# Performance work log

Measured on AMD Instinct MI355X. Metric: run time of the kernel, lower is better.

## Reference

```python
import jax, jax.numpy as jnp
import numpy as np

N, IN_DIM, OUT_DIM, H = 4096, 128, 128, 4
HEAD_DIM = OUT_DIM // H
NEG_SLOPE = 0.2


def setup_inputs() -> dict:
    key = jax.random.key(0)
    k1, k2, k3, k4, k5 = jax.random.split(key, 5)
    x = jax.random.normal(k1, (N, IN_DIM), dtype=jnp.float32)
    adj = jax.random.randint(k2, (N, N), 0, 2, dtype=jnp.int32)
    # nn.Linear(in_dim, out_dim, bias=False): weight is [out_dim, in_dim]
    W = jax.random.normal(k3, (OUT_DIM, IN_DIM), dtype=jnp.float32) * (1.0 / np.sqrt(IN_DIM))
    attn_src = jax.random.normal(k4, (1, H, HEAD_DIM), dtype=jnp.float32) * 0.1
    attn_dst = jax.random.normal(k5, (1, H, HEAD_DIM), dtype=jnp.float32) * 0.1
    return {"x": x, "adj": adj, "W": W, "attn_src": attn_src, "attn_dst": attn_dst}


def reference(x, adj, W, attn_src, attn_dst):
    n = x.shape[0]
    h = (x @ W.T).reshape(n, H, HEAD_DIM)            # [N, H, D]
    e_src = jnp.sum(h * attn_src, axis=-1)           # [N, H]
    e_dst = jnp.sum(h * attn_dst, axis=-1)           # [N, H]
    e = e_src[:, None, :] + e_dst[None, :, :]        # [N, N, H]
    e = jax.nn.leaky_relu(e, negative_slope=NEG_SLOPE)
    e = jnp.where((adj == 0)[:, :, None], -jnp.inf, e)
    alpha = jax.nn.softmax(e, axis=1)                # softmax over neighbors j
    # dropout omitted (eval mode)
    out = jnp.einsum('ijh,jhd->ihd', alpha, h)       # [N, H, D]
    return out.reshape(n, -1)
```

## Files before the change

kernel.cpp:

```cpp
#include <hip/hip_runtime.h>
#include <hip/hip_bf16.h>

#define NN 4096
#define SJ 8
#define JCH (NN / SJ)
#define JSTEP 64
#define NSTEPS (JCH / JSTEP)
#define LOG2E 1.44269504f

typedef __attribute__((ext_vector_type(4))) float f32x4;
typedef __attribute__((ext_vector_type(4))) int i32x4;
typedef __attribute__((ext_vector_type(4))) unsigned int u32x4;
typedef __attribute__((ext_vector_type(8))) short short8;

__device__ __forceinline__ unsigned pk2(float a, float b) {
    float2 t; t.x = a; t.y = b;
    __hip_bfloat162 h = __float22bfloat162_rn(t);
    unsigned r;
    __builtin_memcpy(&r, &h, 4);
    return r;
}

__device__ __forceinline__ short8 load8_bf(const float* __restrict__ p) {
    f32x4 a = *(const f32x4*)p;
    f32x4 b = *(const f32x4*)(p + 4);
    u32x4 v = {pk2(a[0], a[1]), pk2(a[2], a[3]), pk2(b[0], b[1]), pk2(b[2], b[3])};
    return __builtin_bit_cast(short8, v);
}

__global__ __launch_bounds__(256) void k1_proj(
        const float* __restrict__ x, const float* __restrict__ W,
        const float* __restrict__ asrc, const float* __restrict__ adst,
        unsigned short* __restrict__ hT, float* __restrict__ esT,
        float* __restrict__ edT) {
    const int ibase = blockIdx.x * 16;
    const int w = threadIdx.x >> 6;
    const int lane = threadIdx.x & 63;
    const int grp = lane >> 4, li = lane & 15;

    const float* xrow = x + (ibase + li) * 128;
    const float* w0 = W + (w * 32 + li) * 128;
    const float* w1 = W + (w * 32 + 16 + li) * 128;

    f32x4 c0 = {0.f, 0.f, 0.f, 0.f}, c1 = {0.f, 0.f, 0.f, 0.f};
#pragma unroll
    for (int ko = 0; ko < 128; ko += 32) {
        const int kk = ko + grp * 8;
        short8 a = load8_bf(xrow + kk);
        short8 b0 = load8_bf(w0 + kk);
        short8 b1 = load8_bf(w1 + kk);
        c0 = __builtin_amdgcn_mfma_f32_16x16x32_bf16(a, b0, c0, 0, 0, 0);
        c1 = __builtin_amdgcn_mfma_f32_16x16x32_bf16(a, b1, c1, 0, 0, 0);
    }
    const float as0 = asrc[w * 32 + li], as1 = asrc[w * 32 + 16 + li];
    const float ad0 = adst[w * 32 + li], ad1 = adst[w * 32 + 16 + li];
    float pes[4], ped[4];
#pragma unroll
    for (int r = 0; r < 4; ++r) {
        pes[r] = c0[r] * as0 + c1[r] * as1;
        ped[r] = c0[r] * ad0 + c1[r] * ad1;
    }
#pragma unroll
    for (int m = 1; m < 16; m <<= 1) {
#pragma unroll
        for (int r = 0; r < 4; ++r) {
            pes[r] += __shfl_xor(pes[r], m);
            ped[r] += __shfl_xor(ped[r], m);
        }
    }
    if (li == 0) {
#pragma unroll
        for (int r = 0; r < 4; ++r) {
            const int row = ibase + grp * 4 + r;
            esT[w * NN + row] = pes[r] * LOG2E;
            edT[w * NN + row] = ped[r] * LOG2E;
        }
    }
#pragma unroll
    for (int r = 0; r < 4; ++r) {
        const int row = ibase + grp * 4 + r;
        hT[(w * 32 + li) * NN + row] = (unsigned short)__builtin_bit_cast(unsigned short, __float2bfloat16(c0[r]));
        hT[(w * 32 + 16 + li) * NN + row] = (unsigned short)__builtin_bit_cast(unsigned short, __float2bfloat16(c1[r]));
    }
}

__device__ __forceinline__ short8 buildA(float es, const f32x4 edlo, const f32x4 edhi,
                                         const i32x4 alo, const i32x4 ahi) {
    float p[8];
#pragma unroll
    for (int e = 0; e < 4; ++e) {
        float s = es + edlo[e];
        float v = __builtin_amdgcn_exp2f(fmaxf(s, 0.2f * s));
        p[e] = (alo[e] != 0) ? v : 0.0f;
    }
#pragma unroll
    for (int e = 0; e < 4; ++e) {
        float s = es + edhi[e];
        float v = __builtin_amdgcn_exp2f(fmaxf(s, 0.2f * s));
        p[4 + e] = (ahi[e] != 0) ? v : 0.0f;
    }
    u32x4 u = {pk2(p[0], p[1]), pk2(p[2], p[3]), pk2(p[4], p[5]), pk2(p[6], p[7])};
    return __builtin_bit_cast(short8, u);
}

__global__ __launch_bounds__(256) void k3_main(
        const int* __restrict__ adj, const unsigned short* __restrict__ hT,
        const float* __restrict__ esT, const float* __restrict__ edT,
        float* __restrict__ numer, float* __restrict__ denom) {
    __shared__ unsigned int adjbuf[2][32 * 64];

    const int ibase = blockIdx.x * 32;
    const int jstart = blockIdx.y * JCH;
    const int head = threadIdx.x >> 6;
    const int lane = threadIdx.x & 63;
    const int grp = lane >> 4, li = lane & 15;
    const int sub = lane >> 4, p = lane & 15;

    const float es0 = esT[head * NN + ibase + li];
    const float es1 = esT[head * NN + ibase + 16 + li];
    const float* edp = edT + head * NN;
    const unsigned short* h0 = hT + (head * 32 + li) * NN;
    const unsigned short* h1 = hT + (head * 32 + 16 + li) * NN;
    const unsigned int* adju = (const unsigned int*)adj;

    f32x4 c00 = {0.f,0.f,0.f,0.f}, c01 = {0.f,0.f,0.f,0.f};
    f32x4 c10 = {0.f,0.f,0.f,0.f}, c11 = {0.f,0.f,0.f,0.f};
    f32x4 dn0 = {0.f,0.f,0.f,0.f}, dn1 = {0.f,0.f,0.f,0.f};
    short8 bones;
#pragma unroll
    for (int e = 0; e < 8; ++e) bones[e] = (short)0x3F80;

    auto stage = [&](unsigned int* dst, int jb) {
#pragma unroll
        for (int k = 0; k < 2; ++k) {
            const int R = head * 8 + k * 4 + sub;
            const int c = p ^ (R & 15);
            const unsigned int* g = adju + (size_t)(ibase + R) * NN + jb + c * 4;
            __builtin_amdgcn_global_load_lds(g, dst + (head * 8 + k * 4) * 64, 16, 0, 0);
        }
    };

    unsigned int* cur = &adjbuf[0][0];
    unsigned int* nxt = &adjbuf[1][0];

    stage(cur, jstart);
    __syncthreads();

    for (int t = 0; t < NSTEPS; ++t) {
        const int jb = jstart + t * JSTEP;
        if (t + 1 < NSTEPS) stage(nxt, jb + JSTEP);

#pragma unroll
        for (int ks = 0; ks < 2; ++ks) {
            const int j0 = jb + ks * 32 + grp * 8;
            const f32x4 e0 = *(const f32x4*)(edp + j0);
            const f32x4 e1 = *(const f32x4*)(edp + j0 + 4);
            const short8 b0 = *(const short8*)(h0 + j0);
            const short8 b1 = *(const short8*)(h1 + j0);

            const int c0i = ks * 8 + grp * 2;
            const i32x4 q00 = *(const i32x4*)&cur[li * 64 + (c0i ^ li) * 4];
            const i32x4 q01 = *(const i32x4*)&cur[li * 64 + ((c0i + 1) ^ li) * 4];
            const i32x4 q10 = *(const i32x4*)&cur[(li + 16) * 64 + (c0i ^ li) * 4];
            const i32x4 q11 = *(const i32x4*)&cur[(li + 16) * 64 + ((c0i + 1) ^ li) * 4];

            const short8 A0 = buildA(es0, e0, e1, q00, q01);
            const short8 A1 = buildA(es1, e0, e1, q10, q11);

            c00 = __builtin_amdgcn_mfma_f32_16x16x32_bf16(A0, b0, c00, 0, 0, 0);
            c01 = __builtin_amdgcn_mfma_f32_16x16x32_bf16(A0, b1, c01, 0, 0, 0);
            c10 = __builtin_amdgcn_mfma_f32_16x16x32_bf16(A1, b0, c10, 0, 0, 0);
            c11 = __builtin_amdgcn_mfma_f32_16x16x32_bf16(A1, b1, c11, 0, 0, 0);
            dn0 = __builtin_amdgcn_mfma_f32_16x16x32_bf16(A0, bones, dn0, 0, 0, 0);
            dn1 = __builtin_amdgcn_mfma_f32_16x16x32_bf16(A1, bones, dn1, 0, 0, 0);
        }

        __syncthreads();
        unsigned int* tmp = cur; cur = nxt; nxt = tmp;
    }

    const int r0 = ibase + grp * 4;
    float* nb = numer + head * 32 + li;
#pragma unroll
    for (int r = 0; r < 4; ++r) {
        atomicAdd(nb + (size_t)(r0 + r) * 128, c00[r]);
        atomicAdd(nb + (size_t)(r0 + r) * 128 + 16, c01[r]);
        atomicAdd(nb + (size_t)(r0 + 16 + r) * 128, c10[r]);
        atomicAdd(nb + (size_t)(r0 + 16 + r) * 128 + 16, c11[r]);
    }
    if (li == 0) {
#pragma unroll
        for (int r = 0; r < 4; ++r) {
            atomicAdd(denom + (r0 + r) * 4 + head, dn0[r]);
            atomicAdd(denom + (r0 + 16 + r) * 4 + head, dn1[r]);
        }
    }
}

__global__ __launch_bounds__(256) void k4_fin(const float* __restrict__ numer,
                                              const float* __restrict__ denom,
                                              float* __restrict__ out) {
    const int idx = blockIdx.x * 256 + threadIdx.x;
    const int node = idx >> 7;
    const int headc = (idx & 127) >> 5;
    out[idx] = numer[idx] / denom[node * 4 + headc];
}

extern "C" void kernel_launch(void* const* d_in, const int* in_sizes, int n_in,
                              void* d_out, int out_size, void* d_ws, size_t ws_size,
                              hipStream_t stream) {
    const float* x = (const float*)d_in[0];
    const int* adj = (const int*)d_in[1];
    const float* W = (const float*)d_in[2];
    const float* asrc = (const float*)d_in[3];
    const float* adst = (const float*)d_in[4];
    float* out = (float*)d_out;

    char* ws = (char*)d_ws;
    float* numer = (float*)ws;
    float* denom = (float*)(ws + (size_t)2097152);
    float* esT = (float*)(ws + (size_t)2097152 + 65536);
    float* edT = (float*)(ws + (size_t)2097152 + 131072);
    unsigned short* hT = (unsigned short*)(ws + (size_t)2097152 + 196608);

    (void)hipMemsetAsync(numer, 0, 2097152 + 65536, stream);
    k1_proj<<<256, 256, 0, stream>>>(x, W, asrc, adst, hT, esT, edT);
    k3_main<<<dim3(128, SJ), 256, 0, stream>>>(adj, hT, esT, edT, numer, denom);
    k4_fin<<<2048, 256, 0, stream>>>(numer, denom, out);
}
```

Measured before the change: 59.36 us.

## Factor leaky-relu exponent into per-node exp terms, remove per-edge exp2

The per-edge exp2(leaky(es+ed)) becomes max(exp(ed), exp(-0.8 es) * exp(0.2 ed)) multiplied by a row scale. This relies on exp being monotone, and the softmax ratio cancels the constant factor exp(es). The exponentials are computed once per node in the projection kernel, so the inner loop does one multiply, one max and a bitmask select in place of an exp. The adjacency select becomes a bit-AND mask. The j-split also doubles to 16 and occupancy is hinted at 6 waves. In exchange there are extra loads of two per-node arrays, more atomics, and possible overflow or underflow, since exp values are not shifted by a running max.

```diff
diff --git a/kernel.cpp b/kernel.cpp
--- a/kernel.cpp
+++ b/kernel.cpp
@@ -2,7 +2,7 @@
 #include <hip/hip_bf16.h>
 
 #define NN 4096
-#define SJ 8
+#define SJ 16
 #define JCH (NN / SJ)
 #define JSTEP 64
 #define NSTEPS (JCH / JSTEP)
@@ -31,8 +31,8 @@
 __global__ __launch_bounds__(256) void k1_proj(
         const float* __restrict__ x, const float* __restrict__ W,
         const float* __restrict__ asrc, const float* __restrict__ adst,
-        unsigned short* __restrict__ hT, float* __restrict__ esT,
-        float* __restrict__ edT) {
+        unsigned short* __restrict__ hT, float* __restrict__ Rt,
+        float* __restrict__ Bt, float* __restrict__ Dt) {
     const int ibase = blockIdx.x * 16;
     const int w = threadIdx.x >> 6;
     const int lane = threadIdx.x & 63;
@@ -72,8 +72,9 @@
 #pragma unroll
         for (int r = 0; r < 4; ++r) {
             const int row = ibase + grp * 4 + r;
-            esT[w * NN + row] = pes[r] * LOG2E;
-            edT[w * NN + row] = ped[r] * LOG2E;
+            Rt[w * NN + row] = __builtin_amdgcn_exp2f(-0.8f * LOG2E * pes[r]);
+            Bt[w * NN + row] = __builtin_amdgcn_exp2f(LOG2E * ped[r]);
+            Dt[w * NN + row] = __builtin_amdgcn_exp2f(0.2f * LOG2E * ped[r]);
         }
     }
 #pragma unroll
@@ -84,28 +85,31 @@
     }
 }
 
-__device__ __forceinline__ short8 buildA(float es, const f32x4 edlo, const f32x4 edhi,
+__device__ __forceinline__ short8 buildQ(float R,
+                                         const f32x4 B0, const f32x4 B1,
+                                         const f32x4 D0, const f32x4 D1,
                                          const i32x4 alo, const i32x4 ahi) {
     float p[8];
 #pragma unroll
     for (int e = 0; e < 4; ++e) {
-        float s = es + edlo[e];
-        float v = __builtin_amdgcn_exp2f(fmaxf(s, 0.2f * s));
-        p[e] = (alo[e] != 0) ? v : 0.0f;
+        float m = fmaxf(B0[e], R * D0[e]);
+        unsigned bits = __builtin_bit_cast(unsigned, m) & (0u - (unsigned)alo[e]);
+        p[e] = __builtin_bit_cast(float, bits);
     }
 #pragma unroll
     for (int e = 0; e < 4; ++e) {
-        float s = es + edhi[e];
-        float v = __builtin_amdgcn_exp2f(fmaxf(s, 0.2f * s));
-        p[4 + e] = (ahi[e] != 0) ? v : 0.0f;
+        float m = fmaxf(B1[e], R * D1[e]);
+        unsigned bits = __builtin_bit_cast(unsigned, m) & (0u - (unsigned)ahi[e]);
+        p[4 + e] = __builtin_bit_cast(float, bits);
     }
     u32x4 u = {pk2(p[0], p[1]), pk2(p[2], p[3]), pk2(p[4], p[5]), pk2(p[6], p[7])};
     return __builtin_bit_cast(short8, u);
 }
 
-__global__ __launch_bounds__(256) void k3_main(
+__global__ __launch_bounds__(256, 6) void k3_main(
         const int* __restrict__ adj, const unsigned short* __restrict__ hT,
-        const float* __restrict__ esT, const float* __restrict__ edT,
+        const float* __restrict__ Rt, const float* __restrict__ Bt,
+        const float* __restrict__ Dt,
         float* __restrict__ numer, float* __restrict__ denom) {
     __shared__ unsigned int adjbuf[2][32 * 64];
 
@@ -116,9 +120,10 @@
     const int grp = lane >> 4, li = lane & 15;
     const int sub = lane >> 4, p = lane & 15;
 
-    const float es0 = esT[head * NN + ibase + li];
-    const float es1 = esT[head * NN + ibase + 16 + li];
-    const float* edp = edT + head * NN;
+    const float R0 = Rt[head * NN + ibase + li];
+    const float R1 = Rt[head * NN + ibase + 16 + li];
+    const float* Bp = Bt + head * NN;
+    const float* Dp = Dt + head * NN;
     const unsigned short* h0 = hT + (head * 32 + li) * NN;
     const unsigned short* h1 = hT + (head * 32 + 16 + li) * NN;
     const unsigned int* adju = (const unsigned int*)adj;
@@ -153,8 +158,10 @@
 #pragma unroll
         for (int ks = 0; ks < 2; ++ks) {
             const int j0 = jb + ks * 32 + grp * 8;
-            const f32x4 e0 = *(const f32x4*)(edp + j0);
-            const f32x4 e1 = *(const f32x4*)(edp + j0 + 4);
+            const f32x4 Bv0 = *(const f32x4*)(Bp + j0);
+            const f32x4 Bv1 = *(const f32x4*)(Bp + j0 + 4);
+            const f32x4 Dv0 = *(const f32x4*)(Dp + j0);
+            const f32x4 Dv1 = *(const f32x4*)(Dp + j0 + 4);
             const short8 b0 = *(const short8*)(h0 + j0);
             const short8 b1 = *(const short8*)(h1 + j0);
 
@@ -164,8 +171,8 @@
             const i32x4 q10 = *(const i32x4*)&cur[(li + 16) * 64 + (c0i ^ li) * 4];
             const i32x4 q11 = *(const i32x4*)&cur[(li + 16) * 64 + ((c0i + 1) ^ li) * 4];
 
-            const short8 A0 = buildA(es0, e0, e1, q00, q01);
-            const short8 A1 = buildA(es1, e0, e1, q10, q11);
+            const short8 A0 = buildQ(R0, Bv0, Bv1, Dv0, Dv1, q00, q01);
+            const short8 A1 = buildQ(R1, Bv0, Bv1, Dv0, Dv1, q10, q11);
 
             c00 = __builtin_amdgcn_mfma_f32_16x16x32_bf16(A0, b0, c00, 0, 0, 0);
             c01 = __builtin_amdgcn_mfma_f32_16x16x32_bf16(A0, b1, c01, 0, 0, 0);
@@ -219,12 +226,13 @@
     char* ws = (char*)d_ws;
     float* numer = (float*)ws;
     float* denom = (float*)(ws + (size_t)2097152);
-    float* esT = (float*)(ws + (size_t)2097152 + 65536);
-    float* edT = (float*)(ws + (size_t)2097152 + 131072);
-    unsigned short* hT = (unsigned short*)(ws + (size_t)2097152 + 196608);
+    float* Rt = (float*)(ws + (size_t)2097152 + 65536);
+    float* Bt = (float*)(ws + (size_t)2097152 + 131072);
+    float* Dt = (float*)(ws + (size_t)2097152 + 196608);
+    unsigned short* hT = (unsigned short*)(ws + (size_t)2097152 + 262144);
 
     (void)hipMemsetAsync(numer, 0, 2097152 + 65536, stream);
-    k1_proj<<<256, 256, 0, stream>>>(x, W, asrc, adst, hT, esT, edT);
-    k3_main<<<dim3(128, SJ), 256, 0, stream>>>(adj, hT, esT, edT, numer, denom);
+    k1_proj<<<256, 256, 0, stream>>>(x, W, asrc, adst, hT, Rt, Bt, Dt);
+    k3_main<<<dim3(128, SJ), 256, 0, stream>>>(adj, hT, Rt, Bt, Dt, numer, denom);
     k4_fin<<<2048, 256, 0, stream>>>(numer, denom, out);
 }
```

Result: slower. 115.7 us (+94.9%).

## Factor exp of leaky-relu scores, triple-buffer adjacency, prefetch h tiles one step ahead

Applied to the files above, without the earlier changes.

Uses exp(leaky(s+d)) = exp(s)*max(exp(d), exp(-0.8 s)*exp(0.2 d)) with the unnormalized exp(s) row factor cancelling in the softmax. The projection kernel therefore precomputes per-node factors (R = exp(-0.8 es), with B = exp(ed) and D = exp(0.2 ed) packed as bf16), and the main loop needs only a multiply, a max and a mask instead of one exp2 per edge. The adjacency staging becomes a three-buffer ring with explicit vmcnt waits, and the h and factor tiles are loaded into registers one step ahead. The projection also transposes h through LDS so the global stores are coalesced. The trade is bf16 precision for the exponentials, a risk of overflow when unnormalized exponentials are large, and higher register and LDS use.

```diff
diff --git a/kernel.cpp b/kernel.cpp
--- a/kernel.cpp
+++ b/kernel.cpp
@@ -31,8 +31,9 @@
 __global__ __launch_bounds__(256) void k1_proj(
         const float* __restrict__ x, const float* __restrict__ W,
         const float* __restrict__ asrc, const float* __restrict__ adst,
-        unsigned short* __restrict__ hT, float* __restrict__ esT,
-        float* __restrict__ edT) {
+        unsigned short* __restrict__ hT, float* __restrict__ Rt,
+        unsigned* __restrict__ BDt) {
+    __shared__ unsigned short ttile[4][32][16];
     const int ibase = blockIdx.x * 16;
     const int w = threadIdx.x >> 6;
     const int lane = threadIdx.x & 63;
@@ -72,32 +73,48 @@
 #pragma unroll
         for (int r = 0; r < 4; ++r) {
             const int row = ibase + grp * 4 + r;
-            esT[w * NN + row] = pes[r] * LOG2E;
-            edT[w * NN + row] = ped[r] * LOG2E;
-        }
-    }
-#pragma unroll
-    for (int r = 0; r < 4; ++r) {
-        const int row = ibase + grp * 4 + r;
-        hT[(w * 32 + li) * NN + row] = (unsigned short)__builtin_bit_cast(unsigned short, __float2bfloat16(c0[r]));
-        hT[(w * 32 + 16 + li) * NN + row] = (unsigned short)__builtin_bit_cast(unsigned short, __float2bfloat16(c1[r]));
-    }
-}
-
-__device__ __forceinline__ short8 buildA(float es, const f32x4 edlo, const f32x4 edhi,
+            Rt[w * NN + row] = __builtin_amdgcn_exp2f(-0.8f * LOG2E * pes[r]);
+            const float Bv = __builtin_amdgcn_exp2f(LOG2E * ped[r]);
+            const float Dv = __builtin_amdgcn_exp2f(0.2f * LOG2E * ped[r]);
+            BDt[w * NN + row] = pk2(Bv, Dv);
+        }
+    }
+    unsigned short* tw = &ttile[w][0][0];
+    {
+        uint2 v0; v0.x = pk2(c0[0], c0[1]); v0.y = pk2(c0[2], c0[3]);
+        uint2 v1; v1.x = pk2(c1[0], c1[1]); v1.y = pk2(c1[2], c1[3]);
+        *(uint2*)&tw[li * 16 + grp * 4] = v0;
+        *(uint2*)&tw[(li + 16) * 16 + grp * 4] = v1;
+    }
+    __syncthreads();
+    const int d = lane >> 1, half = lane & 1;
+    u32x4 v = *(const u32x4*)&ttile[w][d][half * 8];
+    *(u32x4*)(hT + (size_t)(w * 32 + d) * NN + ibase + half * 8) = v;
+}
+
+struct SR {
+    short8 t00, t01, t10, t11;
+    u32x4 b0a, b0b, b1a, b1b;
+};
+
+__device__ __forceinline__ short8 buildQ(float R, const u32x4 ba, const u32x4 bb,
                                          const i32x4 alo, const i32x4 ahi) {
     float p[8];
 #pragma unroll
     for (int e = 0; e < 4; ++e) {
-        float s = es + edlo[e];
-        float v = __builtin_amdgcn_exp2f(fmaxf(s, 0.2f * s));
-        p[e] = (alo[e] != 0) ? v : 0.0f;
+        const unsigned v = ba[e];
+        const float B = __builtin_bit_cast(float, v << 16);
+        const float D = __builtin_bit_cast(float, v & 0xFFFF0000u);
+        const float m = fmaxf(B, R * D);
+        p[e] = __builtin_bit_cast(float, __builtin_bit_cast(unsigned, m) & (0u - (unsigned)alo[e]));
     }
 #pragma unroll
     for (int e = 0; e < 4; ++e) {
-        float s = es + edhi[e];
-        float v = __builtin_amdgcn_exp2f(fmaxf(s, 0.2f * s));
-        p[4 + e] = (ahi[e] != 0) ? v : 0.0f;
+        const unsigned v = bb[e];
+        const float B = __builtin_bit_cast(float, v << 16);
+        const float D = __builtin_bit_cast(float, v & 0xFFFF0000u);
+        const float m = fmaxf(B, R * D);
+        p[4 + e] = __builtin_bit_cast(float, __builtin_bit_cast(unsigned, m) & (0u - (unsigned)ahi[e]));
     }
     u32x4 u = {pk2(p[0], p[1]), pk2(p[2], p[3]), pk2(p[4], p[5]), pk2(p[6], p[7])};
     return __builtin_bit_cast(short8, u);
@@ -105,9 +122,9 @@
 
 __global__ __launch_bounds__(256) void k3_main(
         const int* __restrict__ adj, const unsigned short* __restrict__ hT,
-        const float* __restrict__ esT, const float* __restrict__ edT,
+        const float* __restrict__ Rt, const unsigned* __restrict__ BDt,
         float* __restrict__ numer, float* __restrict__ denom) {
-    __shared__ unsigned int adjbuf[2][32 * 64];
+    __shared__ unsigned int adjbuf[3][32 * 64];
 
     const int ibase = blockIdx.x * 32;
     const int jstart = blockIdx.y * JCH;
@@ -116,11 +133,11 @@
     const int grp = lane >> 4, li = lane & 15;
     const int sub = lane >> 4, p = lane & 15;
 
-    const float es0 = esT[head * NN + ibase + li];
-    const float es1 = esT[head * NN + ibase + 16 + li];
-    const float* edp = edT + head * NN;
-    const unsigned short* h0 = hT + (head * 32 + li) * NN;
-    const unsigned short* h1 = hT + (head * 32 + 16 + li) * NN;
+    const float R0 = Rt[head * NN + ibase + li];
+    const float R1 = Rt[head * NN + ibase + 16 + li];
+    const unsigned short* h0 = hT + (size_t)(head * 32 + li) * NN;
+    const unsigned short* h1 = hT + (size_t)(head * 32 + 16 + li) * NN;
+    const unsigned* bd = BDt + head * NN;
     const unsigned int* adju = (const unsigned int*)adj;
 
     f32x4 c00 = {0.f,0.f,0.f,0.f}, c01 = {0.f,0.f,0.f,0.f};
@@ -133,50 +150,68 @@
     auto stage = [&](unsigned int* dst, int jb) {
 #pragma unroll
         for (int k = 0; k < 2; ++k) {
-            const int R = head * 8 + k * 4 + sub;
-            const int c = p ^ (R & 15);
-            const unsigned int* g = adju + (size_t)(ibase + R) * NN + jb + c * 4;
+            const int Rw = head * 8 + k * 4 + sub;
+            const int c = p ^ (Rw & 15);
+            const unsigned int* g = adju + (size_t)(ibase + Rw) * NN + jb + c * 4;
             __builtin_amdgcn_global_load_lds(g, dst + (head * 8 + k * 4) * 64, 16, 0, 0);
         }
     };
-
-    unsigned int* cur = &adjbuf[0][0];
-    unsigned int* nxt = &adjbuf[1][0];
-
-    stage(cur, jstart);
-    __syncthreads();
+    auto loadR = [&](int jb) {
+        SR r;
+        r.t00 = *(const short8*)(h0 + jb + grp * 8);
+        r.t01 = *(const short8*)(h0 + jb + 32 + grp * 8);
+        r.t10 = *(const short8*)(h1 + jb + grp * 8);
+        r.t11 = *(const short8*)(h1 + jb + 32 + grp * 8);
+        r.b0a = *(const u32x4*)(bd + jb + grp * 8);
+        r.b0b = *(const u32x4*)(bd + jb + grp * 8 + 4);
+        r.b1a = *(const u32x4*)(bd + jb + 32 + grp * 8);
+        r.b1b = *(const u32x4*)(bd + jb + 32 + grp * 8 + 4);
+        return r;
+    };
+
+    unsigned int* bA = &adjbuf[0][0];
+    unsigned int* bB = &adjbuf[1][0];
+    unsigned int* bC = &adjbuf[2][0];
+
+    stage(bA, jstart);
+    SR Rg = loadR(jstart);
+    stage(bB, jstart + JSTEP);
+    asm volatile("s_waitcnt vmcnt(2)" ::: "memory");
+    __builtin_amdgcn_s_barrier();
 
     for (int t = 0; t < NSTEPS; ++t) {
         const int jb = jstart + t * JSTEP;
-        if (t + 1 < NSTEPS) stage(nxt, jb + JSTEP);
+        SR Rn = Rg;
+        if (t + 1 < NSTEPS) Rn = loadR(jb + JSTEP);
+        if (t + 2 < NSTEPS) stage(bC, jb + 2 * JSTEP);
 
 #pragma unroll
         for (int ks = 0; ks < 2; ++ks) {
-            const int j0 = jb + ks * 32 + grp * 8;
-            const f32x4 e0 = *(const f32x4*)(edp + j0);
-            const f32x4 e1 = *(const f32x4*)(edp + j0 + 4);
-            const short8 b0 = *(const short8*)(h0 + j0);
-            const short8 b1 = *(const short8*)(h1 + j0);
-
-            const int c0i = ks * 8 + grp * 2;
-            const i32x4 q00 = *(const i32x4*)&cur[li * 64 + (c0i ^ li) * 4];
-            const i32x4 q01 = *(const i32x4*)&cur[li * 64 + ((c0i + 1) ^ li) * 4];
-            const i32x4 q10 = *(const i32x4*)&cur[(li + 16) * 64 + (c0i ^ li) * 4];
-            const i32x4 q11 = *(const i32x4*)&cur[(li + 16) * 64 + ((c0i + 1) ^ li) * 4];
-
-            const short8 A0 = buildA(es0, e0, e1, q00, q01);
-            const short8 A1 = buildA(es1, e0, e1, q10, q11);
-
-            c00 = __builtin_amdgcn_mfma_f32_16x16x32_bf16(A0, b0, c00, 0, 0, 0);
-            c01 = __builtin_amdgcn_mfma_f32_16x16x32_bf16(A0, b1, c01, 0, 0, 0);
-            c10 = __builtin_amdgcn_mfma_f32_16x16x32_bf16(A1, b0, c10, 0, 0, 0);
-            c11 = __builtin_amdgcn_mfma_f32_16x16x32_bf16(A1, b1, c11, 0, 0, 0);
+            const short8 tA = ks ? Rg.t01 : Rg.t00;
+            const short8 tB = ks ? Rg.t11 : Rg.t10;
+            const u32x4 ba = ks ? Rg.b1a : Rg.b0a;
+            const u32x4 bb = ks ? Rg.b1b : Rg.b0b;
+            const int cb = ks * 8 + grp * 2;
+            const i32x4 q00 = *(const i32x4*)&bA[li * 64 + (cb ^ li) * 4];
+            const i32x4 q01 = *(const i32x4*)&bA[li * 64 + ((cb + 1) ^ li) * 4];
+            const i32x4 q10 = *(const i32x4*)&bA[(li + 16) * 64 + (cb ^ li) * 4];
+            const i32x4 q11 = *(const i32x4*)&bA[(li + 16) * 64 + ((cb + 1) ^ li) * 4];
+
+            const short8 A0 = buildQ(R0, ba, bb, q00, q01);
+            const short8 A1 = buildQ(R1, ba, bb, q10, q11);
+
+            c00 = __builtin_amdgcn_mfma_f32_16x16x32_bf16(A0, tA, c00, 0, 0, 0);
+            c01 = __builtin_amdgcn_mfma_f32_16x16x32_bf16(A0, tB, c01, 0, 0, 0);
+            c10 = __builtin_amdgcn_mfma_f32_16x16x32_bf16(A1, tA, c10, 0, 0, 0);
+            c11 = __builtin_amdgcn_mfma_f32_16x16x32_bf16(A1, tB, c11, 0, 0, 0);
             dn0 = __builtin_amdgcn_mfma_f32_16x16x32_bf16(A0, bones, dn0, 0, 0, 0);
             dn1 = __builtin_amdgcn_mfma_f32_16x16x32_bf16(A1, bones, dn1, 0, 0, 0);
         }
 
-        __syncthreads();
-        unsigned int* tmp = cur; cur = nxt; nxt = tmp;
+        asm volatile("s_waitcnt vmcnt(2)" ::: "memory");
+        __builtin_amdgcn_s_barrier();
+        unsigned int* tmp = bA; bA = bB; bB = bC; bC = tmp;
+        Rg = Rn;
     }
 
     const int r0 = ibase + grp * 4;
@@ -219,12 +254,12 @@
     char* ws = (char*)d_ws;
     float* numer = (float*)ws;
     float* denom = (float*)(ws + (size_t)2097152);
-    float* esT = (float*)(ws + (size_t)2097152 + 65536);
-    float* edT = (float*)(ws + (size_t)2097152 + 131072);
+    float* Rt = (float*)(ws + (size_t)2097152 + 65536);
+    unsigned* BDt = (unsigned*)(ws + (size_t)2097152 + 131072);
     unsigned short* hT = (unsigned short*)(ws + (size_t)2097152 + 196608);
 
     (void)hipMemsetAsync(numer, 0, 2097152 + 65536, stream);
-    k1_proj<<<256, 256, 0, stream>>>(x, W, asrc, adst, hT, esT, edT);
-    k3_main<<<dim3(128, SJ), 256, 0, stream>>>(adj, hT, esT, edT, numer, denom);
+    k1_proj<<<256, 256, 0, stream>>>(x, W, asrc, adst, hT, Rt, BDt);
+    k3_main<<<dim3(128, SJ), 256, 0, stream>>>(adj, hT, Rt, BDt, numer, denom);
     k4_fin<<<2048, 256, 0, stream>>>(numer, denom, out);
 }
```

New measurement: 57.93 us. 2.4% less time.
